# Kernel optimization log

Measured on AMD Instinct MI355X. Metric: run time of the kernel, lower is better.

The kernel has to match this reference:

```python
import jax, jax.numpy as jnp
import numpy as np

B, D, H, S = 65536, 256, 4, 64
HD = D // H  # head_dim = 64
EPS = 1e-8


def _lin(x, W, b):
    # torch nn.Linear: y = x @ W.T + b, W: [out, in]
    return x @ W.T + b


def _cos_attn(q_heads, keys, vals):
    # q_heads: [B,H,hd]; keys/vals: [H,S,hd] (shared across batch)
    qn = q_heads / (jnp.linalg.norm(q_heads, axis=-1, keepdims=True) + EPS)
    kn = keys / (jnp.linalg.norm(keys, axis=-1, keepdims=True) + EPS)
    sim = jnp.einsum('bhd,hsd->bhs', qn, kn)          # cosine sims, temp=1.0
    attn = jax.nn.softmax(sim, axis=-1)
    return jnp.einsum('bhs,hsd->bhd', attn, vals)     # [B,H,hd]


def setup_inputs() -> dict:
    key = jax.random.key(0)
    ks = jax.random.split(key, 20)

    def xavier(k, shape):
        fan_in, fan_out = shape[1], shape[0]
        lim = np.sqrt(6.0 / (fan_in + fan_out))
        return jax.random.uniform(k, shape, jnp.float32, -lim, lim)

    return {
        'query': jax.random.normal(ks[0], (B, D), jnp.float32),
        'context': jax.random.normal(ks[1], (B, D), jnp.float32),
        'fast_keys': 0.01 * jax.random.normal(ks[2], (H, S, HD), jnp.float32),
        'fast_vals': 0.01 * jax.random.normal(ks[3], (H, S, HD), jnp.float32),
        'deep_keys': 0.01 * jax.random.normal(ks[4], (H, S, HD), jnp.float32),
        'deep_vals': 0.01 * jax.random.normal(ks[5], (H, S, HD), jnp.float32),
        'Wq': xavier(ks[6], (D, D)), 'bq': jnp.zeros((D,), jnp.float32),
        'Wg': xavier(ks[7], (D, D)), 'bg': jnp.zeros((D,), jnp.float32),
        'Wc1': xavier(ks[8], (D // 2, D)), 'bc1': jnp.zeros((D // 2,), jnp.float32),
        'Wc2': xavier(ks[9], (1, D // 2)), 'bc2': jnp.zeros((1,), jnp.float32),
        'Wo': xavier(ks[10], (D, D)), 'bo': jnp.zeros((D,), jnp.float32),
        'Ws': xavier(ks[11], (D, D)), 'bs': jnp.zeros((D,), jnp.float32),
        'mix_logit': jnp.zeros((), jnp.float32),
        'surprise_mean': jnp.zeros((1, D), jnp.float32),
        'surprise_var': jnp.ones((1, D), jnp.float32),
    }


def reference(query, context, fast_keys, fast_vals, deep_keys, deep_vals,
              Wq, bq, Wg, bg, Wc1, bc1, Wc2, bc2, Wo, bo, Ws, bs,
              mix_logit, surprise_mean, surprise_var):
    # --- query projection and head split ---
    q = _lin(query, Wq, bq)                       # [B, D]
    q_heads = q.reshape(B, H, HD)                 # [B, H, hd]

    # --- dual-tier cosine-similarity attention reads ---
    v_fast = _cos_attn(q_heads, fast_keys, fast_vals).reshape(B, D)
    v_deep = _cos_attn(q_heads, deep_keys, deep_vals).reshape(B, D)

    # --- context-gated mixing of tiers ---
    gate = jnp.tanh(_lin(context, Wg, bg)).mean(axis=-1, keepdims=True)  # [B,1]
    mix = jax.nn.sigmoid(mix_logit + gate)
    out = mix * v_fast + (1.0 - mix) * v_deep

    # --- adaptive retrieval confidence head ---
    conf = jax.nn.sigmoid(_lin(jnp.tanh(_lin(context, Wc1, bc1)), Wc2, bc2))  # [B,1]
    out = out * conf
    out = _lin(out, Wo, bo)                       # [B, d_value]

    # --- surprise (detached diagnostic, does not feed output) ---
    h = jax.lax.stop_gradient(_lin(context, Ws, bs))
    z = (h - surprise_mean) / jnp.sqrt(surprise_var + 1e-6)
    surprise = jax.nn.sigmoid(jnp.abs(z).mean(axis=-1) - 2.0)  # 1/max(0.5,0.1)=2.0
    del surprise  # aux diagnostic; main output is the retrieved vector
    return out
```

## Files before the change

### kernel.cpp

```cpp
#include <hip/hip_runtime.h>

typedef unsigned short u16;
typedef __attribute__((ext_vector_type(8))) short bf16x8;
typedef __attribute__((ext_vector_type(4))) float f32x4;
typedef __attribute__((ext_vector_type(4))) unsigned short u16x4;
typedef __attribute__((ext_vector_type(8))) unsigned short u16x8;

#define MFMA16(a, b, c) __builtin_amdgcn_mfma_f32_16x16x32_bf16((a), (b), (c), 0, 0, 0)

#define OFF_WQ   0
#define OFF_WG   65536
#define OFF_WC1  131072
#define OFF_WO   163840
#define OFF_KNF  229376
#define OFF_VTF  245760
#define OFF_KND  262144
#define OFF_VTD  278528

__device__ __forceinline__ u16 f2b(float f) {
  union { float f; unsigned u; } v; v.f = f;
  unsigned r = v.u + 0x7fffu + ((v.u >> 16) & 1u);
  return (u16)(r >> 16);
}
__device__ __forceinline__ float fsig(float x) {
  return __builtin_amdgcn_rcpf(1.f + __expf(-x));
}
__device__ __forceinline__ float ftanh(float x) {
  float e = __expf(2.f * x);
  return (e - 1.f) * __builtin_amdgcn_rcpf(e + 1.f);
}
__device__ __forceinline__ float sum16(float v) {
  v += __shfl_xor(v, 1);
  v += __shfl_xor(v, 2);
  v += __shfl_xor(v, 4);
  v += __shfl_xor(v, 8);
  return v;
}

__global__ void k_prep(const float* __restrict__ Wq, const float* __restrict__ Wg,
                       const float* __restrict__ Wc1, const float* __restrict__ Wo,
                       const float* __restrict__ fk, const float* __restrict__ fv,
                       const float* __restrict__ dk, const float* __restrict__ dv,
                       u16* __restrict__ ws) {
  const int bid = blockIdx.x, t = threadIdx.x;
  if (bid < 96) {
    const float* W = bid < 32 ? Wq : (bid < 64 ? Wg : Wo);
    const int OFF = bid < 32 ? OFF_WQ : (bid < 64 ? OFF_WG : OFF_WO);
    int c = (bid & 31) * 256 + t;
    int lane = c & 63, nt = (c >> 6) & 1, kk = (c >> 7) & 7, w = c >> 10;
    const float* s = W + (w * 32 + nt * 16 + (lane & 15)) * 256 + kk * 32 + ((lane >> 4) & 3) * 8;
    u16x8 o;
    #pragma unroll
    for (int j = 0; j < 8; ++j) o[j] = f2b(s[j]);
    *(u16x8*)(ws + OFF + c * 8) = o;
  } else if (bid < 112) {
    int c = (bid - 96) * 256 + t;
    int lane = c & 63, kk = (c >> 6) & 7, w = c >> 9;
    const float* s = Wc1 + (w * 16 + (lane & 15)) * 256 + kk * 32 + ((lane >> 4) & 3) * 8;
    u16x8 o;
    #pragma unroll
    for (int j = 0; j < 8; ++j) o[j] = f2b(s[j]);
    *(u16x8*)(ws + OFF_WC1 + c * 8) = o;
  } else {
    int idx = (bid - 112) * 256 + t;
    int st = idx >> 8, rowid = idx & 255;
    int h = rowid >> 6, s = rowid & 63;
    if (st < 2) {
      const float* p = (st == 0 ? fk : dk) + rowid * 64;
      const int OFF = (st == 0) ? OFF_KNF : OFF_KND;
      float ss = 0.f;
      #pragma unroll
      for (int d = 0; d < 64; ++d) { float x = p[d]; ss += x * x; }
      float sc = __builtin_amdgcn_rcpf(__builtin_amdgcn_sqrtf(ss) + 1e-8f);
      int nt = s >> 4, sl = s & 15;
      #pragma unroll
      for (int d = 0; d < 64; ++d) {
        int lane = ((d >> 3) & 3) * 16 + sl;
        ws[OFF + (((h * 2 + (d >> 5)) * 4 + nt) * 64 + lane) * 8 + (d & 7)] = f2b(p[d] * sc);
      }
    } else {
      const float* p = (st == 2 ? fv : dv) + rowid * 64;
      const int OFF = (st == 2) ? OFF_VTF : OFF_VTD;
      int kk = s >> 5, quad = (s >> 3) & 3, j = s & 7;
      #pragma unroll
      for (int d = 0; d < 64; ++d) {
        int lane = quad * 16 + (d & 15);
        ws[OFF + (((h * 2 + kk) * 4 + (d >> 4)) * 64 + lane) * 8 + j] = f2b(p[d]);
      }
    }
  }
}

__global__ __launch_bounds__(512, 4)
void k_fused(const float* __restrict__ query, const float* __restrict__ context,
             const float* __restrict__ bq, const float* __restrict__ bg,
             const float* __restrict__ bc1, const float* __restrict__ Wc2,
             const float* __restrict__ bc2v, const float* __restrict__ bo,
             const float* __restrict__ mixl, const u16* __restrict__ ws,
             float* __restrict__ outp) {
  __shared__ u16 sX[64 * 256];
  __shared__ float red_a[8][64];
  __shared__ float red_c[8][64];
  __shared__ float sA[64];
  __shared__ float sB[64];

  const int t = threadIdx.x;
  const int w = t >> 6;
  const int lane = t & 63;
  const int quad = lane >> 4;
  const int l16 = lane & 15;
  const int row4 = quad * 4;
  const int h = w >> 1;
  const int rh = (w & 1) * 32;
  const int blk = blockIdx.x;
  char* Xb = (char*)sX;
  char* Ch = Xb + h * 8192;

  auto stage = [&](const float* src) {
    #pragma unroll
    for (int i = 0; i < 8; ++i) {
      int e = i * 2048 + t * 4;
      float4 v = *(const float4*)(src + e);
      int row = e >> 8, col = e & 255;
      u16x4 pk;
      pk.x = f2b(v.x); pk.y = f2b(v.y); pk.z = f2b(v.z); pk.w = f2b(v.w);
      *(u16x4*)(Xb + row * 512 + ((((col >> 3) ^ (row & 7)) << 4) | ((col & 7) << 1))) = pk;
    }
  };
  auto ldA = [&](int row, int kb) {
    return *(const bf16x8*)(Xb + row * 512 + ((((kb >> 3) ^ (row & 7)) << 4)));
  };
  auto ldC = [&](int row, int kb) {
    return *(const bf16x8*)(Ch + row * 128 + ((((kb >> 3) ^ (row & 7)) << 4)));
  };
  auto cwr = [&](int row, int col, u16 v) {
    *(u16*)(Ch + row * 128 + (((((col >> 3) ^ (row & 7)) << 3) | (col & 7)) << 1)) = v;
  };

  const f32x4 vzero = {0.f, 0.f, 0.f, 0.f};

  stage(context + (size_t)blk * 16384);
  float bgv[2], bqv[2], bov[2];
  #pragma unroll
  for (int nt = 0; nt < 2; ++nt) {
    int n = w * 32 + nt * 16 + l16;
    bgv[nt] = bg[n]; bqv[nt] = bq[n]; bov[nt] = bo[n];
  }
  float bc1v = bc1[w * 16 + l16];
  float wc2v = Wc2[w * 16 + l16];
  __syncthreads();

  {
    f32x4 ag[4][2], ac[4];
    #pragma unroll
    for (int mt = 0; mt < 4; ++mt) { ag[mt][0] = vzero; ag[mt][1] = vzero; ac[mt] = vzero; }
    #pragma unroll
    for (int kk = 0; kk < 8; ++kk) {
      int kb = kk * 32 + quad * 8;
      bf16x8 a0 = ldA(l16, kb), a1 = ldA(16 + l16, kb), a2 = ldA(32 + l16, kb), a3 = ldA(48 + l16, kb);
      #pragma unroll
      for (int nt = 0; nt < 2; ++nt) {
        bf16x8 b = *(const bf16x8*)(ws + OFF_WG + (((w * 8 + kk) * 2 + nt) * 64 + lane) * 8);
        ag[0][nt] = MFMA16(a0, b, ag[0][nt]);
        ag[1][nt] = MFMA16(a1, b, ag[1][nt]);
        ag[2][nt] = MFMA16(a2, b, ag[2][nt]);
        ag[3][nt] = MFMA16(a3, b, ag[3][nt]);
      }
      bf16x8 bc = *(const bf16x8*)(ws + OFF_WC1 + ((w * 8 + kk) * 64 + lane) * 8);
      ac[0] = MFMA16(a0, bc, ac[0]);
      ac[1] = MFMA16(a1, bc, ac[1]);
      ac[2] = MFMA16(a2, bc, ac[2]);
      ac[3] = MFMA16(a3, bc, ac[3]);
    }
    #pragma unroll
    for (int mt = 0; mt < 4; ++mt)
      #pragma unroll
      for (int r = 0; r < 4; ++r) {
        float sg = ftanh(ag[mt][0][r] + bgv[0]) + ftanh(ag[mt][1][r] + bgv[1]);
        sg = sum16(sg);
        float sc = ftanh(ac[mt][r] + bc1v) * wc2v;
        sc = sum16(sc);
        if (l16 == 0) { red_a[w][mt * 16 + row4 + r] = sg; red_c[w][mt * 16 + row4 + r] = sc; }
      }
  }
  __syncthreads();

  if (t < 64) {
    float g = 0.f, cc = 0.f;
    #pragma unroll
    for (int i = 0; i < 8; ++i) { g += red_a[i][t]; cc += red_c[i][t]; }
    float mix = fsig(mixl[0] + g * (1.f / 256.f));
    float conf = fsig(cc + bc2v[0]);
    sA[t] = conf * mix;
    sB[t] = conf - conf * mix;
  }
  stage(query + (size_t)blk * 16384);
  __syncthreads();

  f32x4 qa[4][2];
  {
    #pragma unroll
    for (int mt = 0; mt < 4; ++mt) { qa[mt][0] = vzero; qa[mt][1] = vzero; }
    #pragma unroll
    for (int kk = 0; kk < 8; ++kk) {
      int kb = kk * 32 + quad * 8;
      bf16x8 a0 = ldA(l16, kb), a1 = ldA(16 + l16, kb), a2 = ldA(32 + l16, kb), a3 = ldA(48 + l16, kb);
      #pragma unroll
      for (int nt = 0; nt < 2; ++nt) {
        bf16x8 b = *(const bf16x8*)(ws + OFF_WQ + (((w * 8 + kk) * 2 + nt) * 64 + lane) * 8);
        qa[0][nt] = MFMA16(a0, b, qa[0][nt]);
        qa[1][nt] = MFMA16(a1, b, qa[1][nt]);
        qa[2][nt] = MFMA16(a2, b, qa[2][nt]);
        qa[3][nt] = MFMA16(a3, b, qa[3][nt]);
      }
    }
    #pragma unroll
    for (int mt = 0; mt < 4; ++mt)
      #pragma unroll
      for (int r = 0; r < 4; ++r) {
        float ss = 0.f;
        #pragma unroll
        for (int nt = 0; nt < 2; ++nt) {
          float q_ = qa[mt][nt][r] + bqv[nt];
          qa[mt][nt][r] = q_;
          ss += q_ * q_;
        }
        ss = sum16(ss);
        if (l16 == 0) red_a[w][mt * 16 + row4 + r] = ss;
      }
  }
  __syncthreads();

  #pragma unroll
  for (int mt = 0; mt < 4; ++mt)
    #pragma unroll
    for (int r = 0; r < 4; ++r) {
      int row = mt * 16 + row4 + r;
      float ss = red_a[w][row] + red_a[w ^ 1][row];
      float scl = __builtin_amdgcn_rcpf(__builtin_amdgcn_sqrtf(ss) + 1e-8f);
      #pragma unroll
      for (int nt = 0; nt < 2; ++nt)
        cwr(row, (w & 1) * 32 + nt * 16 + l16, f2b(qa[mt][nt][r] * scl));
    }
  __syncthreads();

  bf16x8 qf[2][2];
  #pragma unroll
  for (int mt = 0; mt < 2; ++mt)
    #pragma unroll
    for (int kk = 0; kk < 2; ++kk)
      qf[mt][kk] = ldC(rh + mt * 16 + l16, kk * 32 + quad * 8);

  f32x4 oacc[2][4];

  #pragma unroll
  for (int tier = 0; tier < 2; ++tier) {
    const u16* KN = ws + (tier == 0 ? OFF_KNF : OFF_KND);
    const u16* VT = ws + (tier == 0 ? OFF_VTF : OFF_VTD);

    f32x4 s[2][4];
    #pragma unroll
    for (int mt = 0; mt < 2; ++mt)
      #pragma unroll
      for (int nt = 0; nt < 4; ++nt) s[mt][nt] = vzero;
    #pragma unroll
    for (int kk = 0; kk < 2; ++kk)
      #pragma unroll
      for (int nt = 0; nt < 4; ++nt) {
        bf16x8 b = *(const bf16x8*)(KN + (((h * 2 + kk) * 4 + nt) * 64 + lane) * 8);
        s[0][nt] = MFMA16(qf[0][kk], b, s[0][nt]);
        s[1][nt] = MFMA16(qf[1][kk], b, s[1][nt]);
      }

    #pragma unroll
    for (int mt = 0; mt < 2; ++mt)
      #pragma unroll
      for (int r = 0; r < 4; ++r) {
        float rs = 0.f;
        #pragma unroll
        for (int nt = 0; nt < 4; ++nt) { float e = __expf(s[mt][nt][r]); s[mt][nt][r] = e; rs += e; }
        rs = sum16(rs);
        float inv = __builtin_amdgcn_rcpf(rs);
        int row = rh + mt * 16 + row4 + r;
        #pragma unroll
        for (int nt = 0; nt < 4; ++nt) cwr(row, nt * 16 + l16, f2b(s[mt][nt][r] * inv));
      }

    bf16x8 p00 = ldC(rh + l16, quad * 8),      p01 = ldC(rh + l16, 32 + quad * 8);
    bf16x8 p10 = ldC(rh + 16 + l16, quad * 8), p11 = ldC(rh + 16 + l16, 32 + quad * 8);
    f32x4 pv[2][4];
    #pragma unroll
    for (int mt = 0; mt < 2; ++mt)
      #pragma unroll
      for (int nt = 0; nt < 4; ++nt) pv[mt][nt] = vzero;
    #pragma unroll
    for (int kk = 0; kk < 2; ++kk)
      #pragma unroll
      for (int nt = 0; nt < 4; ++nt) {
        bf16x8 b = *(const bf16x8*)(VT + (((h * 2 + kk) * 4 + nt) * 64 + lane) * 8);
        pv[0][nt] = MFMA16(kk ? p01 : p00, b, pv[0][nt]);
        pv[1][nt] = MFMA16(kk ? p11 : p10, b, pv[1][nt]);
      }

    #pragma unroll
    for (int mt = 0; mt < 2; ++mt)
      #pragma unroll
      for (int r = 0; r < 4; ++r) {
        float m_ = (tier == 0) ? sA[rh + mt * 16 + row4 + r] : sB[rh + mt * 16 + row4 + r];
        #pragma unroll
        for (int nt = 0; nt < 4; ++nt) {
          if (tier == 0) oacc[mt][nt][r] = m_ * pv[mt][nt][r];
          else           oacc[mt][nt][r] += m_ * pv[mt][nt][r];
        }
      }
  }

  __syncthreads();
  #pragma unroll
  for (int mt = 0; mt < 2; ++mt)
    #pragma unroll
    for (int r = 0; r < 4; ++r) {
      int row = rh + mt * 16 + row4 + r;
      #pragma unroll
      for (int nt = 0; nt < 4; ++nt) {
        int col = h * 64 + nt * 16 + l16;
        *(u16*)(Xb + row * 512 + ((((col >> 3) ^ (row & 7)) << 4) | ((col & 7) << 1))) =
            f2b(oacc[mt][nt][r]);
      }
    }
  __syncthreads();

  {
    f32x4 o[4][2];
    #pragma unroll
    for (int mt = 0; mt < 4; ++mt) { o[mt][0] = vzero; o[mt][1] = vzero; }
    #pragma unroll
    for (int kk = 0; kk < 8; ++kk) {
      int kb = kk * 32 + quad * 8;
      bf16x8 a0 = ldA(l16, kb), a1 = ldA(16 + l16, kb), a2 = ldA(32 + l16, kb), a3 = ldA(48 + l16, kb);
      #pragma unroll
      for (int nt = 0; nt < 2; ++nt) {
        bf16x8 b = *(const bf16x8*)(ws + OFF_WO + (((w * 8 + kk) * 2 + nt) * 64 + lane) * 8);
        o[0][nt] = MFMA16(a0, b, o[0][nt]);
        o[1][nt] = MFMA16(a1, b, o[1][nt]);
        o[2][nt] = MFMA16(a2, b, o[2][nt]);
        o[3][nt] = MFMA16(a3, b, o[3][nt]);
      }
    }
    float* dst = outp + (size_t)blk * 16384;
    #pragma unroll
    for (int mt = 0; mt < 4; ++mt)
      #pragma unroll
      for (int r = 0; r < 4; ++r) {
        int row = mt * 16 + row4 + r;
        #pragma unroll
        for (int nt = 0; nt < 2; ++nt)
          dst[row * 256 + w * 32 + nt * 16 + l16] = o[mt][nt][r] + bov[nt];
      }
  }
}

extern "C" void kernel_launch(void* const* d_in, const int* in_sizes, int n_in,
                              void* d_out, int out_size, void* d_ws, size_t ws_size,
                              hipStream_t stream) {
  const float* query   = (const float*)d_in[0];
  const float* context = (const float*)d_in[1];
  const float* fk      = (const float*)d_in[2];
  const float* fv      = (const float*)d_in[3];
  const float* dk      = (const float*)d_in[4];
  const float* dv      = (const float*)d_in[5];
  const float* Wq      = (const float*)d_in[6];
  const float* bq      = (const float*)d_in[7];
  const float* Wg      = (const float*)d_in[8];
  const float* bg      = (const float*)d_in[9];
  const float* Wc1     = (const float*)d_in[10];
  const float* bc1     = (const float*)d_in[11];
  const float* Wc2     = (const float*)d_in[12];
  const float* bc2     = (const float*)d_in[13];
  const float* Wo      = (const float*)d_in[14];
  const float* bo      = (const float*)d_in[15];
  const float* mixl    = (const float*)d_in[18];
  u16* ws = (u16*)d_ws;
  float* outp = (float*)d_out;

  k_prep<<<116, 256, 0, stream>>>(Wq, Wg, Wc1, Wo, fk, fv, dk, dv, ws);
  k_fused<<<1024, 512, 0, stream>>>(query, context, bq, bg, bc1, Wc2, bc2, bo,
                                    mixl, ws, outp);
}
```

Measured before the change: 294.9 us.

## Double-buffer query and context staging in LDS and split attention by row halves

Adds a second 32KB LDS buffer so query and context are both loaded and converted up front, which removes the barrier and load stall between the gate GEMM and the query GEMM. Attention is processed in two 16-row halves to lower register pressure, and its output goes into the second buffer, which drops one barrier. bf16 packing now uses the v_cvt_pk_bf16_f32 instruction. LDS use roughly doubles to about 70KB per block, which likely cuts the number of resident 512-thread blocks per CU below the launch-bounds target of 4.

```diff
diff --git a/kernel.cpp b/kernel.cpp
--- a/kernel.cpp
+++ b/kernel.cpp
@@ -21,6 +21,11 @@
   union { float f; unsigned u; } v; v.f = f;
   unsigned r = v.u + 0x7fffu + ((v.u >> 16) & 1u);
   return (u16)(r >> 16);
+}
+__device__ __forceinline__ unsigned pk2(float lo, float hi) {
+  unsigned r;
+  asm("v_cvt_pk_bf16_f32 %0, %1, %2" : "=v"(r) : "v"(lo), "v"(hi));
+  return r;
 }
 __device__ __forceinline__ float fsig(float x) {
   return __builtin_amdgcn_rcpf(1.f + __expf(-x));
@@ -99,8 +104,10 @@
              const float* __restrict__ mixl, const u16* __restrict__ ws,
              float* __restrict__ outp) {
   __shared__ u16 sX[64 * 256];
+  __shared__ u16 sY[64 * 256];
   __shared__ float red_a[8][64];
   __shared__ float red_c[8][64];
+  __shared__ float red_q[8][64];
   __shared__ float sA[64];
   __shared__ float sB[64];
 
@@ -114,21 +121,23 @@
   const int rh = (w & 1) * 32;
   const int blk = blockIdx.x;
   char* Xb = (char*)sX;
+  char* Yb = (char*)sY;
   char* Ch = Xb + h * 8192;
 
-  auto stage = [&](const float* src) {
+  auto stage = [&](char* dstB, const float* src) {
     #pragma unroll
     for (int i = 0; i < 8; ++i) {
       int e = i * 2048 + t * 4;
       float4 v = *(const float4*)(src + e);
       int row = e >> 8, col = e & 255;
-      u16x4 pk;
-      pk.x = f2b(v.x); pk.y = f2b(v.y); pk.z = f2b(v.z); pk.w = f2b(v.w);
-      *(u16x4*)(Xb + row * 512 + ((((col >> 3) ^ (row & 7)) << 4) | ((col & 7) << 1))) = pk;
-    }
-  };
-  auto ldA = [&](int row, int kb) {
-    return *(const bf16x8*)(Xb + row * 512 + ((((kb >> 3) ^ (row & 7)) << 4)));
+      uint2 pk;
+      pk.x = pk2(v.x, v.y);
+      pk.y = pk2(v.z, v.w);
+      *(uint2*)(dstB + row * 512 + ((((col >> 3) ^ (row & 7)) << 4) | ((col & 7) << 1))) = pk;
+    }
+  };
+  auto ldA = [&](const char* B, int row, int kb) {
+    return *(const bf16x8*)(B + row * 512 + ((((kb >> 3) ^ (row & 7)) << 4)));
   };
   auto ldC = [&](int row, int kb) {
     return *(const bf16x8*)(Ch + row * 128 + ((((kb >> 3) ^ (row & 7)) << 4)));
@@ -136,10 +145,14 @@
   auto cwr = [&](int row, int col, u16 v) {
     *(u16*)(Ch + row * 128 + (((((col >> 3) ^ (row & 7)) << 3) | (col & 7)) << 1)) = v;
   };
+  auto ywr = [&](int row, int col, u16 v) {
+    *(u16*)(Yb + row * 512 + (((((col >> 3) ^ (row & 7)) << 3) | (col & 7)) << 1)) = v;
+  };
 
   const f32x4 vzero = {0.f, 0.f, 0.f, 0.f};
 
-  stage(context + (size_t)blk * 16384);
+  stage(Xb, context + (size_t)blk * 16384);
+  stage(Yb, query + (size_t)blk * 16384);
   float bgv[2], bqv[2], bov[2];
   #pragma unroll
   for (int nt = 0; nt < 2; ++nt) {
@@ -157,7 +170,8 @@
     #pragma unroll
     for (int kk = 0; kk < 8; ++kk) {
       int kb = kk * 32 + quad * 8;
-      bf16x8 a0 = ldA(l16, kb), a1 = ldA(16 + l16, kb), a2 = ldA(32 + l16, kb), a3 = ldA(48 + l16, kb);
+      bf16x8 a0 = ldA(Xb, l16, kb), a1 = ldA(Xb, 16 + l16, kb),
+             a2 = ldA(Xb, 32 + l16, kb), a3 = ldA(Xb, 48 + l16, kb);
       #pragma unroll
       for (int nt = 0; nt < 2; ++nt) {
         bf16x8 b = *(const bf16x8*)(ws + OFF_WG + (((w * 8 + kk) * 2 + nt) * 64 + lane) * 8);
@@ -194,9 +208,6 @@
     sA[t] = conf * mix;
     sB[t] = conf - conf * mix;
   }
-  stage(query + (size_t)blk * 16384);
-  __syncthreads();
-
   f32x4 qa[4][2];
   {
     #pragma unroll
@@ -204,7 +215,8 @@
     #pragma unroll
     for (int kk = 0; kk < 8; ++kk) {
       int kb = kk * 32 + quad * 8;
-      bf16x8 a0 = ldA(l16, kb), a1 = ldA(16 + l16, kb), a2 = ldA(32 + l16, kb), a3 = ldA(48 + l16, kb);
+      bf16x8 a0 = ldA(Yb, l16, kb), a1 = ldA(Yb, 16 + l16, kb),
+             a2 = ldA(Yb, 32 + l16, kb), a3 = ldA(Yb, 48 + l16, kb);
       #pragma unroll
       for (int nt = 0; nt < 2; ++nt) {
         bf16x8 b = *(const bf16x8*)(ws + OFF_WQ + (((w * 8 + kk) * 2 + nt) * 64 + lane) * 8);
@@ -226,7 +238,7 @@
           ss += q_ * q_;
         }
         ss = sum16(ss);
-        if (l16 == 0) red_a[w][mt * 16 + row4 + r] = ss;
+        if (l16 == 0) red_q[w][mt * 16 + row4 + r] = ss;
       }
   }
   __syncthreads();
@@ -236,7 +248,7 @@
     #pragma unroll
     for (int r = 0; r < 4; ++r) {
       int row = mt * 16 + row4 + r;
-      float ss = red_a[w][row] + red_a[w ^ 1][row];
+      float ss = red_q[w][row] + red_q[w ^ 1][row];
       float scl = __builtin_amdgcn_rcpf(__builtin_amdgcn_sqrtf(ss) + 1e-8f);
       #pragma unroll
       for (int nt = 0; nt < 2; ++nt)
@@ -244,90 +256,74 @@
     }
   __syncthreads();
 
-  bf16x8 qf[2][2];
   #pragma unroll
-  for (int mt = 0; mt < 2; ++mt)
-    #pragma unroll
-    for (int kk = 0; kk < 2; ++kk)
-      qf[mt][kk] = ldC(rh + mt * 16 + l16, kk * 32 + quad * 8);
-
-  f32x4 oacc[2][4];
-
-  #pragma unroll
-  for (int tier = 0; tier < 2; ++tier) {
-    const u16* KN = ws + (tier == 0 ? OFF_KNF : OFF_KND);
-    const u16* VT = ws + (tier == 0 ? OFF_VTF : OFF_VTD);
-
-    f32x4 s[2][4];
-    #pragma unroll
-    for (int mt = 0; mt < 2; ++mt)
-      #pragma unroll
-      for (int nt = 0; nt < 4; ++nt) s[mt][nt] = vzero;
-    #pragma unroll
-    for (int kk = 0; kk < 2; ++kk)
-      #pragma unroll
-      for (int nt = 0; nt < 4; ++nt) {
-        bf16x8 b = *(const bf16x8*)(KN + (((h * 2 + kk) * 4 + nt) * 64 + lane) * 8);
-        s[0][nt] = MFMA16(qf[0][kk], b, s[0][nt]);
-        s[1][nt] = MFMA16(qf[1][kk], b, s[1][nt]);
-      }
-
-    #pragma unroll
-    for (int mt = 0; mt < 2; ++mt)
+  for (int half = 0; half < 2; ++half) {
+    const int r0 = rh + half * 16;
+    bf16x8 q0 = ldC(r0 + l16, quad * 8);
+    bf16x8 q1 = ldC(r0 + l16, 32 + quad * 8);
+    f32x4 oa[4];
+
+    #pragma unroll
+    for (int tier = 0; tier < 2; ++tier) {
+      const u16* KN = ws + (tier == 0 ? OFF_KNF : OFF_KND);
+      const u16* VT = ws + (tier == 0 ? OFF_VTF : OFF_VTD);
+
+      f32x4 s4[4];
+      #pragma unroll
+      for (int nt = 0; nt < 4; ++nt) s4[nt] = vzero;
+      #pragma unroll
+      for (int kk = 0; kk < 2; ++kk)
+        #pragma unroll
+        for (int nt = 0; nt < 4; ++nt) {
+          bf16x8 b = *(const bf16x8*)(KN + (((h * 2 + kk) * 4 + nt) * 64 + lane) * 8);
+          s4[nt] = MFMA16(kk ? q1 : q0, b, s4[nt]);
+        }
+
       #pragma unroll
       for (int r = 0; r < 4; ++r) {
         float rs = 0.f;
         #pragma unroll
-        for (int nt = 0; nt < 4; ++nt) { float e = __expf(s[mt][nt][r]); s[mt][nt][r] = e; rs += e; }
+        for (int nt = 0; nt < 4; ++nt) { float e = __expf(s4[nt][r]); s4[nt][r] = e; rs += e; }
         rs = sum16(rs);
         float inv = __builtin_amdgcn_rcpf(rs);
-        int row = rh + mt * 16 + row4 + r;
-        #pragma unroll
-        for (int nt = 0; nt < 4; ++nt) cwr(row, nt * 16 + l16, f2b(s[mt][nt][r] * inv));
-      }
-
-    bf16x8 p00 = ldC(rh + l16, quad * 8),      p01 = ldC(rh + l16, 32 + quad * 8);
-    bf16x8 p10 = ldC(rh + 16 + l16, quad * 8), p11 = ldC(rh + 16 + l16, 32 + quad * 8);
-    f32x4 pv[2][4];
-    #pragma unroll
-    for (int mt = 0; mt < 2; ++mt)
-      #pragma unroll
-      for (int nt = 0; nt < 4; ++nt) pv[mt][nt] = vzero;
-    #pragma unroll
-    for (int kk = 0; kk < 2; ++kk)
-      #pragma unroll
-      for (int nt = 0; nt < 4; ++nt) {
-        bf16x8 b = *(const bf16x8*)(VT + (((h * 2 + kk) * 4 + nt) * 64 + lane) * 8);
-        pv[0][nt] = MFMA16(kk ? p01 : p00, b, pv[0][nt]);
-        pv[1][nt] = MFMA16(kk ? p11 : p10, b, pv[1][nt]);
-      }
-
-    #pragma unroll
-    for (int mt = 0; mt < 2; ++mt)
-      #pragma unroll
-      for (int r = 0; r < 4; ++r) {
-        float m_ = (tier == 0) ? sA[rh + mt * 16 + row4 + r] : sB[rh + mt * 16 + row4 + r];
+        int row = r0 + row4 + r;
+        #pragma unroll
+        for (int nt = 0; nt < 4; ++nt) cwr(row, nt * 16 + l16, f2b(s4[nt][r] * inv));
+      }
+
+      bf16x8 p0 = ldC(r0 + l16, quad * 8);
+      bf16x8 p1 = ldC(r0 + l16, 32 + quad * 8);
+      f32x4 pv4[4];
+      #pragma unroll
+      for (int nt = 0; nt < 4; ++nt) pv4[nt] = vzero;
+      #pragma unroll
+      for (int kk = 0; kk < 2; ++kk)
         #pragma unroll
         for (int nt = 0; nt < 4; ++nt) {
-          if (tier == 0) oacc[mt][nt][r] = m_ * pv[mt][nt][r];
-          else           oacc[mt][nt][r] += m_ * pv[mt][nt][r];
+          bf16x8 b = *(const bf16x8*)(VT + (((h * 2 + kk) * 4 + nt) * 64 + lane) * 8);
+          pv4[nt] = MFMA16(kk ? p1 : p0, b, pv4[nt]);
         }
-      }
-  }
-
-  __syncthreads();
-  #pragma unroll
-  for (int mt = 0; mt < 2; ++mt)
+
+      #pragma unroll
+      for (int r = 0; r < 4; ++r) {
+        int row = r0 + row4 + r;
+        float m_ = (tier == 0) ? sA[row] : sB[row];
+        #pragma unroll
+        for (int nt = 0; nt < 4; ++nt) {
+          if (tier == 0) oa[nt][r] = m_ * pv4[nt][r];
+          else           oa[nt][r] += m_ * pv4[nt][r];
+        }
+      }
+    }
+
     #pragma unroll
     for (int r = 0; r < 4; ++r) {
-      int row = rh + mt * 16 + row4 + r;
-      #pragma unroll
-      for (int nt = 0; nt < 4; ++nt) {
-        int col = h * 64 + nt * 16 + l16;
-        *(u16*)(Xb + row * 512 + ((((col >> 3) ^ (row & 7)) << 4) | ((col & 7) << 1))) =
-            f2b(oacc[mt][nt][r]);
-      }
-    }
+      int row = r0 + row4 + r;
+      #pragma unroll
+      for (int nt = 0; nt < 4; ++nt)
+        ywr(row, h * 64 + nt * 16 + l16, f2b(oa[nt][r]));
+    }
+  }
   __syncthreads();
 
   {
@@ -337,7 +333,8 @@
     #pragma unroll
     for (int kk = 0; kk < 8; ++kk) {
       int kb = kk * 32 + quad * 8;
-      bf16x8 a0 = ldA(l16, kb), a1 = ldA(16 + l16, kb), a2 = ldA(32 + l16, kb), a3 = ldA(48 + l16, kb);
+      bf16x8 a0 = ldA(Yb, l16, kb), a1 = ldA(Yb, 16 + l16, kb),
+             a2 = ldA(Yb, 32 + l16, kb), a3 = ldA(Yb, 48 + l16, kb);
       #pragma unroll
       for (int nt = 0; nt < 2; ++nt) {
         bf16x8 b = *(const bf16x8*)(ws + OFF_WO + (((w * 8 + kk) * 2 + nt) * 64 + lane) * 8);
```

Result: faster. 281.3 us (-4.6%).
